# Kernel tuning notes

Hardware: AMD Instinct MI355X
Metric: run time of the kernel (lower is better)

## Reference

```python
import jax, jax.numpy as jnp
import numpy as np

N_QUBITS = 8
EMBED_DIM = 1024
FFN_DIM = 4096


def setup_inputs() -> dict:
    key = jax.random.key(0)
    ks = jax.random.split(key, 6)
    x = jax.random.normal(ks[0], (8, 4096, EMBED_DIM), dtype=jnp.float32)
    # trainable RY rotation angles, one per wire (torchquantum RY has_params=True)
    theta = jax.random.normal(ks[1], (N_QUBITS,), dtype=jnp.float32)
    # torch nn.Linear params: W [out, in], b [out]
    W1 = jax.random.normal(ks[2], (FFN_DIM, N_QUBITS), dtype=jnp.float32) / np.sqrt(N_QUBITS)
    b1 = jnp.zeros((FFN_DIM,), dtype=jnp.float32)
    W2 = jax.random.normal(ks[3], (EMBED_DIM, FFN_DIM), dtype=jnp.float32) / np.sqrt(FFN_DIM)
    b2 = jnp.zeros((EMBED_DIM,), dtype=jnp.float32)
    return {"x": x, "theta": theta, "W1": W1, "b1": b1, "W2": W2, "b2": b2}


def reference(x, theta, W1, b1, W2, b2):
    # Quantum layer: per token, encoder resets state to |0..0>, applies RX(x_i)
    # on wire i, then trainable RY(theta_i), then measures <Z_i>. The circuit has
    # no entangling gates, so it factorizes per wire with the closed form:
    #   <Z_i> = cos(theta_i) * cos(x[..., i])
    # (RY(t)RX(a)|0> gives <Z> = cos t * cos a). Vectorized over batch and seq.
    q = jnp.cos(theta) * jnp.cos(x[..., :N_QUBITS])   # [B, S, n_qubits]
    # dropout is identity in eval mode
    h = jax.nn.relu(jnp.einsum('bsq,fq->bsf', q, W1) + b1)  # [B, S, ffn]
    out = jnp.einsum('bsf,ef->bse', h, W2) + b2              # [B, S, embed]
    return out
```

## Files before the change

kernel.cpp:

```cpp
#include <hip/hip_runtime.h>
#include <cstdint>
#include <cstddef>


#define M_TOT 32768L
#define N_DIM 1024
#define K_DIM 4096
#define BM 256
#define BN 256
#define BK 64
#define NT_K (K_DIM / BK)
#define CM_MAX 16384L

typedef __attribute__((ext_vector_type(8))) short short8;
typedef __attribute__((ext_vector_type(4))) float f32x4;

__device__ __forceinline__ uint16_t f2bf(float f) {
  uint32_t u = __builtin_bit_cast(uint32_t, f);
  uint32_t r = (u + 0x7fffu + ((u >> 16) & 1u)) >> 16;
  return (uint16_t)r;
}

__device__ __forceinline__ void gload_lds16(const void* gsrc, void* ldst) {
  __builtin_amdgcn_global_load_lds(
      (const __attribute__((address_space(1))) void*)gsrc,
      (__attribute__((address_space(3))) void*)ldst, 16, 0, 0);
}

__global__ __launch_bounds__(256) void prep_w2(const float* __restrict__ W2,
                                               uint16_t* __restrict__ W2sw) {
  long idx = (long)blockIdx.x * 256 + threadIdx.x;
  long e8 = idx * 8;
  int e = (int)(e8 >> 12);
  int k = (int)(e8 & 4095);
  float4 v0 = *(const float4*)(W2 + e8);
  float4 v1 = *(const float4*)(W2 + e8 + 4);
  union { uint16_t u[8]; uint4 v; } pk;
  pk.u[0] = f2bf(v0.x); pk.u[1] = f2bf(v0.y); pk.u[2] = f2bf(v0.z); pk.u[3] = f2bf(v0.w);
  pk.u[4] = f2bf(v1.x); pk.u[5] = f2bf(v1.y); pk.u[6] = f2bf(v1.z); pk.u[7] = f2bf(v1.w);
  int sg = ((k >> 3) & 7) ^ (e & 7);
  uint16_t* dst = W2sw + (long)e * 4096 + (k & ~63) + sg * 8;
  *(uint4*)dst = pk.v;
}

__global__ __launch_bounds__(256) void h_kernel(const float* __restrict__ x,
                                                const float* __restrict__ theta,
                                                const float* __restrict__ W1,
                                                const float* __restrict__ b1,
                                                uint16_t* __restrict__ Hsw) {
  __shared__ float qs[64][8];
  int tid = threadIdx.x;
  long m0 = (long)blockIdx.x * 64;
  int g = blockIdx.y * 256 + tid;
  int f0 = g * 8;

  for (int idx = tid; idx < 512; idx += 256) {
    int t = idx >> 3, i = idx & 7;
    qs[t][i] = __cosf(theta[i]) * cosf(x[(m0 + t) * 1024 + i]);
  }
  __syncthreads();

  float4 w[16];
#pragma unroll
  for (int j = 0; j < 8; ++j) {
    w[2 * j]     = *(const float4*)(W1 + (long)(f0 + j) * 8);
    w[2 * j + 1] = *(const float4*)(W1 + (long)(f0 + j) * 8 + 4);
  }
  float bb[8];
#pragma unroll
  for (int j = 0; j < 8; ++j) bb[j] = b1[f0 + j];

  int blk = (g >> 3) * 64;
  int gw = g & 7;

#pragma unroll 2
  for (int t = 0; t < 64; ++t) {
    long m = m0 + t;
    float q0 = qs[t][0], q1 = qs[t][1], q2 = qs[t][2], q3 = qs[t][3];
    float q4 = qs[t][4], q5 = qs[t][5], q6 = qs[t][6], q7 = qs[t][7];
    union { uint16_t u[8]; uint4 v; } pk;
#pragma unroll
    for (int j = 0; j < 8; ++j) {
      float h = bb[j];
      h += q0 * w[2 * j].x + q1 * w[2 * j].y + q2 * w[2 * j].z + q3 * w[2 * j].w;
      h += q4 * w[2 * j + 1].x + q5 * w[2 * j + 1].y + q6 * w[2 * j + 1].z + q7 * w[2 * j + 1].w;
      h = fmaxf(h, 0.0f);
      pk.u[j] = f2bf(h);
    }
    int sg = gw ^ ((int)m & 7);
    *(uint4*)&Hsw[m * K_DIM + blk + sg * 8] = pk.v;
  }
}

__global__ __launch_bounds__(512, 2) void gemm_kernel(const uint16_t* __restrict__ Hsw,
                                                      const uint16_t* __restrict__ W2sw,
                                                      const float* __restrict__ b2,
                                                      float* __restrict__ out) {
  __shared__ uint16_t LA[2 * BM * BK];
  __shared__ uint16_t LB[2 * BN * BK];

  int nwg = gridDim.x;
  int bid = blockIdx.x;
  int sw = bid;
  if ((nwg & 7) == 0) { int cpx = nwg >> 3; sw = (bid & 7) * cpx + (bid >> 3); }
  const int NTN = N_DIM / BN;
  int mt = sw / NTN;
  int nt = sw - mt * NTN;
  long m0 = (long)mt * BM;
  int n0 = nt * BN;

  int tid = threadIdx.x;
  int lane = tid & 63;
  int wave_m = (tid >> 6) >> 2;
  int wave_n = (tid >> 6) & 3;
  int wmB = wave_m * 128;
  int wnB = wave_n * 64;

  int r  = lane & 15;
  int kq = lane >> 4;
  int xr = r & 7;

  int rowS = tid >> 3;
  int colS = (tid & 7) * 8;
  const uint16_t* srcA = Hsw  + (m0 + rowS) * K_DIM + colS;
  const uint16_t* srcB = W2sw + ((long)(n0 + rowS)) * K_DIM + colS;
  int ldsWB = (tid & ~63) * 8;

#define STAGE_A(p, h, j, t) \
  gload_lds16(srcA + (long)((h)*128 + (j)*64) * K_DIM + (t)*BK, \
              &LA[(p)*16384 + ((h)*128 + (j)*64)*BK + ldsWB])
#define STAGE_B(p, h, j, t) \
  gload_lds16(srcB + (long)((h)*128 + (j)*64) * K_DIM + (t)*BK, \
              &LB[(p)*16384 + ((h)*128 + (j)*64)*BK + ldsWB])

#define BAR() do { asm volatile("" ::: "memory"); __builtin_amdgcn_s_barrier(); \
                   asm volatile("" ::: "memory"); } while (0)

#define LDA_F(p, mf_, ks_) \
  (*(const short8*)&LA[(p)*16384 + (wmB + (mf_)*16 + r)*BK + ((((ks_)*4 + kq) ^ xr)*8)])
#define LDB_F(p, nf_, ks_) \
  (*(const short8*)&LB[(p)*16384 + (wnB + (nf_)*16 + r)*BK + ((((ks_)*4 + kq) ^ xr)*8)])

#define MFMA_Q(AARR, BARR, mh, nh) do { \
    __builtin_amdgcn_s_setprio(1); \
    _Pragma("unroll") for (int i_ = 0; i_ < 4; ++i_) \
    _Pragma("unroll") for (int j_ = 0; j_ < 2; ++j_) \
    _Pragma("unroll") for (int ks_ = 0; ks_ < 2; ++ks_) \
      acc[(mh)*4 + i_][(nh)*2 + j_] = __builtin_amdgcn_mfma_f32_16x16x32_bf16( \
          AARR[i_][ks_], BARR[j_][ks_], acc[(mh)*4 + i_][(nh)*2 + j_], 0, 0, 0); \
    __builtin_amdgcn_s_setprio(0); \
  } while (0)

  f32x4 acc[8][4];
#pragma unroll
  for (int i = 0; i < 8; ++i)
#pragma unroll
    for (int j = 0; j < 4; ++j) acc[i][j] = (f32x4){0.f, 0.f, 0.f, 0.f};

  short8 a0[4][2];
  short8 a1[4][2];
  short8 b0[2][2];
  short8 b1v[2][2];

#pragma unroll
  for (int h = 0; h < 2; ++h)
#pragma unroll
    for (int j = 0; j < 2; ++j) STAGE_A(0, h, j, 0);
#pragma unroll
  for (int h = 0; h < 2; ++h)
#pragma unroll
    for (int j = 0; j < 2; ++j) STAGE_B(0, h, j, 0);
#pragma unroll
  for (int h = 0; h < 2; ++h)
#pragma unroll
    for (int j = 0; j < 2; ++j) STAGE_A(1, h, j, 1);
#pragma unroll
  for (int h = 0; h < 2; ++h)
#pragma unroll
    for (int j = 0; j < 2; ++j) STAGE_B(1, h, j, 1);
  asm volatile("s_waitcnt vmcnt(8)" ::: "memory");
  BAR();
#pragma unroll
  for (int i = 0; i < 4; ++i)
#pragma unroll
    for (int ks = 0; ks < 2; ++ks) a0[i][ks] = LDA_F(0, i, ks);
#pragma unroll
  for (int j = 0; j < 2; ++j)
#pragma unroll
    for (int ks = 0; ks < 2; ++ks) b0[j][ks] = LDB_F(0, j, ks);

#pragma unroll 2
  for (int u = 0; u < NT_K; ++u) {
    int p = u & 1;
    bool st = (u < NT_K - 2);
    bool rd = (u < NT_K - 1);

    MFMA_Q(a0, b0, 0, 0);
#pragma unroll
    for (int j = 0; j < 2; ++j)
#pragma unroll
      for (int ks = 0; ks < 2; ++ks) b1v[j][ks] = LDB_F(p, 2 + j, ks);
#pragma unroll
    for (int i = 0; i < 4; ++i)
#pragma unroll
      for (int ks = 0; ks < 2; ++ks) a1[i][ks] = LDA_F(p, 4 + i, ks);
    BAR();

    MFMA_Q(a0, b1v, 0, 1);
    if (st) { STAGE_A(p, 0, 0, u + 2); STAGE_A(p, 1, 0, u + 2); }
    BAR();

    MFMA_Q(a1, b1v, 1, 1);
    if (st) { STAGE_B(p, 0, 0, u + 2); STAGE_B(p, 0, 1, u + 2);
              STAGE_B(p, 1, 0, u + 2); STAGE_B(p, 1, 1, u + 2); }
    if (st)                 { asm volatile("s_waitcnt vmcnt(6)" ::: "memory"); }
    else if (u == NT_K - 2) { asm volatile("s_waitcnt vmcnt(0)" ::: "memory"); }
    BAR();

    MFMA_Q(a1, b0, 1, 0);
    if (rd) {
#pragma unroll
      for (int i = 0; i < 4; ++i)
#pragma unroll
        for (int ks = 0; ks < 2; ++ks) a0[i][ks] = LDA_F(p ^ 1, i, ks);
#pragma unroll
      for (int j = 0; j < 2; ++j)
#pragma unroll
        for (int ks = 0; ks < 2; ++ks) b0[j][ks] = LDB_F(p ^ 1, j, ks);
    }
    if (st) { STAGE_A(p, 0, 1, u + 2); STAGE_A(p, 1, 1, u + 2); }
    BAR();
  }

  float bb[4];
#pragma unroll
  for (int nf = 0; nf < 4; ++nf) bb[nf] = b2[n0 + wnB + nf * 16 + r];
  long mbase = m0 + wmB + kq * 4;
#pragma unroll
  for (int mf = 0; mf < 8; ++mf) {
#pragma unroll
    for (int nf = 0; nf < 4; ++nf) {
      int n = n0 + wnB + nf * 16 + r;
#pragma unroll
      for (int rg = 0; rg < 4; ++rg) {
        out[(mbase + mf * 16 + rg) * N_DIM + n] = acc[mf][nf][rg] + bb[nf];
      }
    }
  }
#undef STAGE_A
#undef STAGE_B
#undef BAR
#undef LDA_F
#undef LDB_F
#undef MFMA_Q
}

extern "C" void kernel_launch(void* const* d_in, const int* in_sizes, int n_in,
                              void* d_out, int out_size, void* d_ws, size_t ws_size,
                              hipStream_t stream) {
  const float* x     = (const float*)d_in[0];
  const float* theta = (const float*)d_in[1];
  const float* W1    = (const float*)d_in[2];
  const float* b1    = (const float*)d_in[3];
  const float* W2    = (const float*)d_in[4];
  const float* b2    = (const float*)d_in[5];
  float* out = (float*)d_out;

  const size_t W2SW_BYTES = (size_t)N_DIM * K_DIM * 2;
  uint16_t* W2sw = (uint16_t*)d_ws;
  uint16_t* Hsw  = (uint16_t*)((char*)d_ws + W2SW_BYTES);

  size_t avail = ws_size > W2SW_BYTES ? ws_size - W2SW_BYTES : 0;
  long CM = (long)(avail / ((size_t)K_DIM * 2));
  CM &= ~255L;
  if (CM > CM_MAX) CM = CM_MAX;
  if (CM < 256) CM = 256;

  prep_w2<<<2048, 256, 0, stream>>>(W2, W2sw);

  for (long m0 = 0; m0 < M_TOT; m0 += CM) {
    long mc = M_TOT - m0;
    if (mc > CM) mc = CM;
    dim3 gA((unsigned)(mc / 64), 2);
    h_kernel<<<gA, 256, 0, stream>>>(x + m0 * N_DIM, theta, W1, b1, Hsw);
    unsigned ngb = (unsigned)((mc / BM) * (N_DIM / BN));
    gemm_kernel<<<ngb, 512, 0, stream>>>(Hsw, W2sw, b2, out + m0 * N_DIM);
  }
}
```

Before: 309.0 us.

## Switch GEMM inner loop to 32x32x16 MFMA with reworked LDS schedule

Replaces the 16x16x32 bf16 MFMA tiles with 32x32x16 MFMA, changing the fragment layout, LDS swizzled read addressing, accumulator shape and epilogue store mapping. The main loop is also restructured: LDS fragment reads now happen at the start of each quarter instead of being prefetched a stage ahead, with extra barriers and lgkmcnt(0) waits before each MFMA group. The goal is fewer MFMA instructions and fewer LDS reads per FLOP. The added barriers and the loss of register prefetch may expose LDS latency.

```diff
diff --git a/kernel.cpp b/kernel.cpp
--- a/kernel.cpp
+++ b/kernel.cpp
@@ -13,7 +13,7 @@
 #define CM_MAX 16384L
 
 typedef __attribute__((ext_vector_type(8))) short short8;
-typedef __attribute__((ext_vector_type(4))) float f32x4;
+typedef __attribute__((ext_vector_type(16))) float f32x16;
 
 __device__ __forceinline__ uint16_t f2bf(float f) {
   uint32_t u = __builtin_bit_cast(uint32_t, f);
@@ -116,9 +116,8 @@
   int wmB = wave_m * 128;
   int wnB = wave_n * 64;
 
-  int r  = lane & 15;
-  int kq = lane >> 4;
-  int xr = r & 7;
+  int r31 = lane & 31;
+  int lh  = lane >> 5;
 
   int rowS = tid >> 3;
   int colS = (tid & 7) * 8;
@@ -135,32 +134,35 @@
 
 #define BAR() do { asm volatile("" ::: "memory"); __builtin_amdgcn_s_barrier(); \
                    asm volatile("" ::: "memory"); } while (0)
-
-#define LDA_F(p, mf_, ks_) \
-  (*(const short8*)&LA[(p)*16384 + (wmB + (mf_)*16 + r)*BK + ((((ks_)*4 + kq) ^ xr)*8)])
-#define LDB_F(p, nf_, ks_) \
-  (*(const short8*)&LB[(p)*16384 + (wnB + (nf_)*16 + r)*BK + ((((ks_)*4 + kq) ^ xr)*8)])
-
-#define MFMA_Q(AARR, BARR, mh, nh) do { \
+#define LG0() do { asm volatile("s_waitcnt lgkmcnt(0)" ::: "memory"); \
+                   __builtin_amdgcn_sched_barrier(0); } while (0)
+
+#define LDA32(p, mtile, ks_) \
+  (*(const short8*)&LA[(p)*16384 + (wmB + (mtile)*32 + r31)*BK + \
+                       ((((ks_)*2 + lh) ^ ((wmB + (mtile)*32 + r31) & 7))*8)])
+#define LDB32(p, ntile, ks_) \
+  (*(const short8*)&LB[(p)*16384 + (wnB + (ntile)*32 + r31)*BK + \
+                       ((((ks_)*2 + lh) ^ ((wnB + (ntile)*32 + r31) & 7))*8)])
+
+#define MFMA_Q(AARR, BV, mh, ntile) do { \
     __builtin_amdgcn_s_setprio(1); \
-    _Pragma("unroll") for (int i_ = 0; i_ < 4; ++i_) \
-    _Pragma("unroll") for (int j_ = 0; j_ < 2; ++j_) \
-    _Pragma("unroll") for (int ks_ = 0; ks_ < 2; ++ks_) \
-      acc[(mh)*4 + i_][(nh)*2 + j_] = __builtin_amdgcn_mfma_f32_16x16x32_bf16( \
-          AARR[i_][ks_], BARR[j_][ks_], acc[(mh)*4 + i_][(nh)*2 + j_], 0, 0, 0); \
+    _Pragma("unroll") for (int i_ = 0; i_ < 2; ++i_) \
+    _Pragma("unroll") for (int ks_ = 0; ks_ < 4; ++ks_) \
+      acc[(mh)*2 + i_][(ntile)] = __builtin_amdgcn_mfma_f32_32x32x16_bf16( \
+          AARR[i_][ks_], BV[ks_], acc[(mh)*2 + i_][(ntile)], 0, 0, 0); \
     __builtin_amdgcn_s_setprio(0); \
   } while (0)
 
-  f32x4 acc[8][4];
-#pragma unroll
-  for (int i = 0; i < 8; ++i)
-#pragma unroll
-    for (int j = 0; j < 4; ++j) acc[i][j] = (f32x4){0.f, 0.f, 0.f, 0.f};
-
-  short8 a0[4][2];
-  short8 a1[4][2];
-  short8 b0[2][2];
-  short8 b1v[2][2];
+  f32x16 acc[4][2];
+#pragma unroll
+  for (int i = 0; i < 4; ++i)
+#pragma unroll
+    for (int j = 0; j < 2; ++j) acc[i][j] = (f32x16)(0.0f);
+
+  short8 a0[2][4];
+  short8 a1[2][4];
+  short8 b0[4];
+  short8 b1v[4];
 
 #pragma unroll
   for (int h = 0; h < 2; ++h)
@@ -180,78 +182,74 @@
     for (int j = 0; j < 2; ++j) STAGE_B(1, h, j, 1);
   asm volatile("s_waitcnt vmcnt(8)" ::: "memory");
   BAR();
-#pragma unroll
-  for (int i = 0; i < 4; ++i)
-#pragma unroll
-    for (int ks = 0; ks < 2; ++ks) a0[i][ks] = LDA_F(0, i, ks);
-#pragma unroll
-  for (int j = 0; j < 2; ++j)
-#pragma unroll
-    for (int ks = 0; ks < 2; ++ks) b0[j][ks] = LDB_F(0, j, ks);
 
 #pragma unroll 2
   for (int u = 0; u < NT_K; ++u) {
     int p = u & 1;
     bool st = (u < NT_K - 2);
-    bool rd = (u < NT_K - 1);
-
+
+#pragma unroll
+    for (int i = 0; i < 2; ++i)
+#pragma unroll
+      for (int ks = 0; ks < 4; ++ks) a0[i][ks] = LDA32(p, i, ks);
+#pragma unroll
+    for (int ks = 0; ks < 4; ++ks) b0[ks] = LDB32(p, 0, ks);
+    asm volatile("s_waitcnt lgkmcnt(8)" ::: "memory");
+    BAR();
+    LG0();
     MFMA_Q(a0, b0, 0, 0);
-#pragma unroll
-    for (int j = 0; j < 2; ++j)
-#pragma unroll
-      for (int ks = 0; ks < 2; ++ks) b1v[j][ks] = LDB_F(p, 2 + j, ks);
-#pragma unroll
-    for (int i = 0; i < 4; ++i)
-#pragma unroll
-      for (int ks = 0; ks < 2; ++ks) a1[i][ks] = LDA_F(p, 4 + i, ks);
-    BAR();
-
+    BAR();
+
+#pragma unroll
+    for (int ks = 0; ks < 4; ++ks) b1v[ks] = LDB32(p, 1, ks);
+    if (st) { STAGE_A(p, 0, 0, u + 2); STAGE_A(p, 1, 0, u + 2); }
+    BAR();
+    LG0();
     MFMA_Q(a0, b1v, 0, 1);
-    if (st) { STAGE_A(p, 0, 0, u + 2); STAGE_A(p, 1, 0, u + 2); }
-    BAR();
-
-    MFMA_Q(a1, b1v, 1, 1);
+    BAR();
+
+#pragma unroll
+    for (int i = 0; i < 2; ++i)
+#pragma unroll
+      for (int ks = 0; ks < 4; ++ks) a1[i][ks] = LDA32(p, 2 + i, ks);
     if (st) { STAGE_B(p, 0, 0, u + 2); STAGE_B(p, 0, 1, u + 2);
               STAGE_B(p, 1, 0, u + 2); STAGE_B(p, 1, 1, u + 2); }
+    BAR();
+    LG0();
+    MFMA_Q(a1, b1v, 1, 1);
     if (st)                 { asm volatile("s_waitcnt vmcnt(6)" ::: "memory"); }
     else if (u == NT_K - 2) { asm volatile("s_waitcnt vmcnt(0)" ::: "memory"); }
     BAR();
 
+    if (st) { STAGE_A(p, 0, 1, u + 2); STAGE_A(p, 1, 1, u + 2); }
+    BAR();
+    LG0();
     MFMA_Q(a1, b0, 1, 0);
-    if (rd) {
-#pragma unroll
-      for (int i = 0; i < 4; ++i)
-#pragma unroll
-        for (int ks = 0; ks < 2; ++ks) a0[i][ks] = LDA_F(p ^ 1, i, ks);
-#pragma unroll
-      for (int j = 0; j < 2; ++j)
-#pragma unroll
-        for (int ks = 0; ks < 2; ++ks) b0[j][ks] = LDB_F(p ^ 1, j, ks);
-    }
-    if (st) { STAGE_A(p, 0, 1, u + 2); STAGE_A(p, 1, 1, u + 2); }
-    BAR();
-  }
-
-  float bb[4];
-#pragma unroll
-  for (int nf = 0; nf < 4; ++nf) bb[nf] = b2[n0 + wnB + nf * 16 + r];
-  long mbase = m0 + wmB + kq * 4;
-#pragma unroll
-  for (int mf = 0; mf < 8; ++mf) {
-#pragma unroll
-    for (int nf = 0; nf < 4; ++nf) {
-      int n = n0 + wnB + nf * 16 + r;
-#pragma unroll
-      for (int rg = 0; rg < 4; ++rg) {
-        out[(mbase + mf * 16 + rg) * N_DIM + n] = acc[mf][nf][rg] + bb[nf];
+    BAR();
+  }
+
+  float bbv[2];
+#pragma unroll
+  for (int ntile = 0; ntile < 2; ++ntile) bbv[ntile] = b2[n0 + wnB + ntile * 32 + r31];
+#pragma unroll
+  for (int mtile = 0; mtile < 4; ++mtile) {
+    long mb = m0 + wmB + mtile * 32 + 4 * lh;
+#pragma unroll
+    for (int ntile = 0; ntile < 2; ++ntile) {
+      int n = n0 + wnB + ntile * 32 + r31;
+#pragma unroll
+      for (int reg = 0; reg < 16; ++reg) {
+        int row = (reg & 3) + 8 * (reg >> 2);
+        out[(mb + row) * N_DIM + n] = acc[mtile][ntile][reg] + bbv[ntile];
       }
     }
   }
 #undef STAGE_A
 #undef STAGE_B
 #undef BAR
-#undef LDA_F
-#undef LDB_F
+#undef LG0
+#undef LDA32
+#undef LDB32
 #undef MFMA_Q
 }
 
```

After: 355.7 us. 1.15x slower.
